# Kernel tuning notes

Hardware: AMD Instinct MI355X
Metric: run time of the kernel (lower is better)

## Reference

```python
import jax, jax.numpy as jnp
import numpy as np

H = 32  # GRU hidden size


def _conv1d(x, w, b, stride, pad):
    # x: (B, Cin, L), w: (Cout, Cin, K)
    y = jax.lax.conv_general_dilated(
        x, w, window_strides=(stride,), padding=[(pad, pad)],
        dimension_numbers=('NCH', 'OIH', 'NCH'))
    return y + b[None, :, None]


def setup_inputs() -> dict:
    key = jax.random.key(0)
    ks = jax.random.split(key, 16)
    B = 16384
    inp = {
        'past_samples': jax.random.normal(ks[0], (B, 2000), jnp.float32),
        'velocity': jax.random.uniform(ks[1], (B,), jnp.float32),
        'log_pitch': jax.random.normal(ks[2], (B,), jnp.float32),
        'time': jax.random.uniform(ks[3], (B,), jnp.float32),
        'hidden_state': jax.random.normal(ks[4], (B, H), jnp.float32),
        # conv stack params
        'w1': jax.random.normal(ks[5], (4, 1, 31), jnp.float32) * 0.1,
        'b1': jnp.zeros((4,), jnp.float32),
        'w2': jax.random.normal(ks[6], (8, 4, 15), jnp.float32) * 0.1,
        'b2': jnp.zeros((8,), jnp.float32),
        'w3': jax.random.normal(ks[7], (16, 8, 7), jnp.float32) * 0.1,
        'b3': jnp.zeros((16,), jnp.float32),
        # GRU params (torch layout: rows = [r; z; n])
        'w_ih': jax.random.normal(ks[8], (3 * H, 19), jnp.float32) * 0.1,
        'w_hh': jax.random.normal(ks[9], (3 * H, H), jnp.float32) * 0.1,
        'b_ih': jnp.zeros((3 * H,), jnp.float32),
        'b_hh': jnp.zeros((3 * H,), jnp.float32),
        # projection
        'w_proj': jax.random.normal(ks[10], (2, H), jnp.float32) * 0.1,
        'b_proj': jnp.zeros((2,), jnp.float32),
    }
    return inp


def reference(past_samples, velocity, log_pitch, time, hidden_state,
              w1, b1, w2, b2, w3, b3, w_ih, w_hh, b_ih, b_hh, w_proj, b_proj):
    x = past_samples[:, None, :]                       # (B,1,2000)
    x = jax.nn.relu(_conv1d(x, w1, b1, 4, 15))         # (B,4,500)
    x = jax.nn.relu(_conv1d(x, w2, b2, 4, 7))          # (B,8,125)
    x = jax.nn.relu(_conv1d(x, w3, b3, 4, 3))          # (B,16,32)
    ctx = jnp.mean(x, axis=2)                          # adaptive avg pool -> (B,16)

    rnn_in = jnp.concatenate(
        [ctx, velocity[:, None], log_pitch[:, None], time[:, None]], axis=1)  # (B,19)

    # single GRU step (torch GRUCell math)
    gi = rnn_in @ w_ih.T + b_ih                        # (B,3H)
    gh = hidden_state @ w_hh.T + b_hh                  # (B,3H)
    r = jax.nn.sigmoid(gi[:, :H] + gh[:, :H])
    z = jax.nn.sigmoid(gi[:, H:2 * H] + gh[:, H:2 * H])
    n = jnp.tanh(gi[:, 2 * H:] + r * gh[:, 2 * H:])
    new_hidden = (1.0 - z) * n + z * hidden_state      # (B,H)

    out = new_hidden @ w_proj.T + b_proj               # (B,2)
    mu, log_sigma = out[:, :1], out[:, 1:]
    sigma = jnp.exp(log_sigma)
    return (mu, sigma, new_hidden)
```

## Files before the change

### kernel.cpp

```cpp
#include <hip/hip_runtime.h>
#include <hip/hip_fp16.h>
#include <math.h>


typedef _Float16 h4 __attribute__((ext_vector_type(4)));
typedef _Float16 h8 __attribute__((ext_vector_type(8)));
typedef float f4 __attribute__((ext_vector_type(4)));

#define PACK_MAG0 0x57A9EDB1u
#define PACK_MAG1 0x1BDE9A75u
#define NITER 5

__device__ __forceinline__ void block_sync_lds()
{
    asm volatile("s_waitcnt lgkmcnt(0)" ::: "memory");
    __builtin_amdgcn_s_barrier();
}
__device__ __forceinline__ void wait_vm0()
{
    asm volatile("s_waitcnt vmcnt(0)" ::: "memory");
}

#if defined(__has_builtin)
#if __has_builtin(__builtin_amdgcn_global_load_lds)
#define HAVE_GLL 1
#endif
#endif

__device__ __forceinline__ void async_ld16(const float* g, float* lds)
{
#ifdef HAVE_GLL
    __builtin_amdgcn_global_load_lds(
        (const __attribute__((address_space(1))) void*)g,
        (__attribute__((address_space(3))) void*)lds, 16, 0, 0);
#else
    const int l = threadIdx.x & 63;
    ((float4*)lds)[l] = *(const float4*)g;
#endif
}

__global__ void pack_weights(const float* __restrict__ w1,
                             const float* __restrict__ w2,
                             const float* __restrict__ w3,
                             const float* __restrict__ w_ih,
                             _Float16* __restrict__ hws,
                             float* __restrict__ wihp,
                             unsigned int* __restrict__ flag)
{
    if (flag[0] == PACK_MAG0 && flag[1] == PACK_MAG1) return;

    for (int i = threadIdx.x; i < 1024; i += 256) {
        int kk = i >> 9, l = (i >> 3) & 63, j = i & 7;
        int m = l & 15, oct = l >> 4;
        int k = kk * 32 + oct * 8 + j;
        int delta = m >> 2, c = m & 3;
        int tap = k - 4 * delta - 1;
        float v = (tap >= 0 && tap < 31) ? w1[c * 31 + tap] : 0.0f;
        hws[i] = (_Float16)v;
    }
    for (int i = threadIdx.x; i < 1024; i += 256) {
        int kk = i >> 9, l = (i >> 3) & 63, j = i & 7;
        int c = l & 15, k = kk * 32 + ((l >> 4) << 3) + j;
        int tap = k >> 2, ci = k & 3;
        float v = (c < 8 && tap < 15) ? w2[(c * 4 + ci) * 15 + tap] : 0.0f;
        hws[1024 + i] = (_Float16)v;
    }
    for (int i = threadIdx.x; i < 1024; i += 256) {
        int kk = i >> 9, l = (i >> 3) & 63, j = i & 7;
        int c = l & 15, k = kk * 32 + ((l >> 4) << 3) + j;
        int tap = k >> 3, ci = k & 7;
        float v = (tap < 7) ? w3[(c * 8 + ci) * 7 + tap] : 0.0f;
        hws[2048 + i] = (_Float16)v;
    }
    for (int idx = threadIdx.x; idx < 96 * 20; idx += 256) {
        int r = idx / 20, c = idx % 20;
        wihp[idx] = (c < 19) ? w_ih[r * 19 + c] : 0.0f;
    }
    __syncthreads();
    if (threadIdx.x == 0) { flag[0] = PACK_MAG0; flag[1] = PACK_MAG1; }
}

__global__ void __launch_bounds__(128, 4)
wavernn_fused(const float* __restrict__ past,
              const float* __restrict__ velocity,
              const float* __restrict__ log_pitch,
              const float* __restrict__ time_in,
              const float* __restrict__ hidden,
              const float* __restrict__ b1,
              const float* __restrict__ b2,
              const float* __restrict__ b3,
              const float* __restrict__ wihp,
              const float* __restrict__ w_hh,
              const float* __restrict__ b_ih, const float* __restrict__ b_hh,
              const float* __restrict__ w_proj, const float* __restrict__ b_proj,
              const _Float16* __restrict__ hws,
              float* __restrict__ out, int B)
{
    __shared__ __align__(16) float regA[2048];
    __shared__ __align__(16) _Float16 regB[2112];
    __shared__ float rnnp[2][16];
    __shared__ float hsl[32];
    __shared__ float rnn3[4];

    float* const raw      = regA;
    _Float16* const y1t   = (_Float16*)regA;
    _Float16* const xbuf  = regB;
    _Float16* const y2t   = regB;
    float* const G        = (float*)regB;

    const h8* const wf1 = (const h8*)hws;
    const h8* const wf2 = (const h8*)(hws + 1024);
    const h8* const wf3 = (const h8*)(hws + 2048);

    const int tid = threadIdx.x;
    const int w   = tid >> 6;
    const int l   = tid & 63;
    const int o   = l >> 4;
    const int q   = l & 15;
    const f4 z4 = {0.0f, 0.0f, 0.0f, 0.0f};

    const int item0 = blockIdx.x * NITER;

    const h8 a10 = wf1[l],      a11 = wf1[64 + l];
    const h8 a20 = wf2[l],      a21 = wf2[64 + l];
    const h8 a30 = wf3[l],      a31 = wf3[64 + l];
    const float bv0 = b1[0], bv1 = b1[1], bv2 = b1[2], bv3 = b1[3];
    float b2v[4], b3v[4];
#pragma unroll
    for (int r = 0; r < 4; ++r) { b2v[r] = b2[(o * 4 + r) & 7];
                                  b3v[r] = b3[o * 4 + r]; }

    if (tid < 96) xbuf[2016 + tid] = (_Float16)0.0f;

    auto stage_issue = [&](int ii) {
        const float* row = past + (size_t)ii * 2000;
#pragma unroll
        for (int c = 0; c < 4; ++c) {
            int foff = w * 1024 + c * 256 + l * 4;
            if (foff > 1996) foff = 1996;
            async_ld16(row + foff, raw + w * 1024 + c * 256);
        }
    };

    stage_issue(item0);

    for (int it = 0; it < NITER; ++it) {
        const int ii = item0 + it;
        if (ii >= B) break;

        wait_vm0();
        if (tid < 32) hsl[tid] = hidden[(size_t)ii * 32 + tid];
        if (tid == 0) { rnn3[0] = velocity[ii];
                        rnn3[1] = log_pitch[ii];
                        rnn3[2] = time_in[ii]; }
        if (tid < 16) xbuf[tid] = (_Float16)0.0f;
        if (tid < 125) {
            const float4* r4 = (const float4*)raw + 4 * tid;
#pragma unroll
            for (int k = 0; k < 4; ++k) {
                float4 v = r4[k];
                h4 hv = {(_Float16)v.x, (_Float16)v.y,
                         (_Float16)v.z, (_Float16)v.w};
                *(h4*)(xbuf + 16 + 16 * tid + 4 * k) = hv;
            }
        }
        block_sync_lds();

        if (tid < 28) y1t[tid] = (_Float16)0.0f;
        else if (tid < 48) y1t[2000 + tid] = (_Float16)0.0f;
#pragma unroll
        for (int Ti = 0; Ti < 4; ++Ti) {
            const int T = 4 * w + Ti;
            h8 x0 = *(const h8*)(xbuf + 256 * T + 16 * q + 8 * o);
            h8 x1 = *(const h8*)(xbuf + 256 * T + 16 * q + 32 + 8 * o);
            f4 d = __builtin_amdgcn_mfma_f32_16x16x32_f16(a10, x0, z4, 0, 0, 0);
            d = __builtin_amdgcn_mfma_f32_16x16x32_f16(a11, x1, d, 0, 0, 0);
            const int p = 64 * T + 4 * q + o;
            if (p < 500) {
                h4 wv = {(_Float16)fmaxf(d[0] + bv0, 0.0f),
                         (_Float16)fmaxf(d[1] + bv1, 0.0f),
                         (_Float16)fmaxf(d[2] + bv2, 0.0f),
                         (_Float16)fmaxf(d[3] + bv3, 0.0f)};
                *(h4*)(y1t + (7 + p) * 4) = wv;
            }
        }
        block_sync_lds();

        if (tid < 24) y2t[tid] = (_Float16)0.0f;
        if (tid >= 96) y2t[928 + tid] = (_Float16)0.0f;
#pragma unroll
        for (int Ti = 0; Ti < 4; ++Ti) {
            const int T = 4 * w + Ti;
            const int p = T * 16 + q;
            h8 x0 = *(const h8*)(y1t + 16 * p + 8 * o);
            h8 x1 = *(const h8*)(y1t + 16 * p + 32 + 8 * o);
            f4 d = __builtin_amdgcn_mfma_f32_16x16x32_f16(a20, x0, z4, 0, 0, 0);
            d = __builtin_amdgcn_mfma_f32_16x16x32_f16(a21, x1, d, 0, 0, 0);
            if (o < 2 && p < 125) {
                h4 wv = {(_Float16)fmaxf(d[0] + b2v[0], 0.0f),
                         (_Float16)fmaxf(d[1] + b2v[1], 0.0f),
                         (_Float16)fmaxf(d[2] + b2v[2], 0.0f),
                         (_Float16)fmaxf(d[3] + b2v[3], 0.0f)};
                *(h4*)(y2t + (3 + p) * 8 + o * 4) = wv;
            }
        }
        block_sync_lds();

        if (it + 1 < NITER && ii + 1 < B) stage_issue(ii + 1);

        {
            const int p = 16 * w + q;
            h8 x0 = *(const h8*)(y2t + 32 * p + 8 * o);
            h8 x1 = *(const h8*)(y2t + 32 * p + 32 + 8 * o);
            f4 d = __builtin_amdgcn_mfma_f32_16x16x32_f16(a30, x0, z4, 0, 0, 0);
            d = __builtin_amdgcn_mfma_f32_16x16x32_f16(a31, x1, d, 0, 0, 0);
#pragma unroll
            for (int r = 0; r < 4; ++r) {
                float v = fmaxf(d[r] + b3v[r], 0.0f);
                v += __shfl_xor(v, 1); v += __shfl_xor(v, 2);
                v += __shfl_xor(v, 4); v += __shfl_xor(v, 8);
                if (q == 0) rnnp[w][o * 4 + r] = v;
            }
        }
        block_sync_lds();

        if (tid < 96) {
            float rv[20];
#pragma unroll
            for (int j = 0; j < 16; ++j)
                rv[j] = (rnnp[0][j] + rnnp[1][j]) * (1.0f / 32.0f);
            rv[16] = rnn3[0]; rv[17] = rnn3[1]; rv[18] = rnn3[2]; rv[19] = 0.0f;

            float a = b_ih[tid];
            const float4* wr = (const float4*)(wihp + tid * 20);
#pragma unroll
            for (int j = 0; j < 5; ++j) {
                float4 qv = wr[j];
                a += rv[4 * j] * qv.x + rv[4 * j + 1] * qv.y +
                     rv[4 * j + 2] * qv.z + rv[4 * j + 3] * qv.w;
            }
            G[tid] = a;

            float hv[32];
#pragma unroll
            for (int j = 0; j < 32; ++j) hv[j] = hsl[j];

            float g = b_hh[tid];
            const float4* wh = (const float4*)(w_hh + tid * 32);
#pragma unroll
            for (int j = 0; j < 8; ++j) {
                float4 qv = wh[j];
                g += hv[4 * j] * qv.x + hv[4 * j + 1] * qv.y +
                     hv[4 * j + 2] * qv.z + hv[4 * j + 3] * qv.w;
            }
            G[96 + tid] = g;
        }
        block_sync_lds();

        if (tid < 32) {
            const int j = tid;
            float r = 1.0f / (1.0f + expf(-(G[j] + G[96 + j])));
            float z = 1.0f / (1.0f + expf(-(G[32 + j] + G[128 + j])));
            float n = tanhf(G[64 + j] + r * G[160 + j]);
            float nh = (1.0f - z) * n + z * hsl[j];
            out[(size_t)2 * B + (size_t)ii * 32 + j] = nh;

            float p0 = nh * w_proj[j];
            float p1 = nh * w_proj[32 + j];
            p0 += __shfl_xor(p0, 16); p1 += __shfl_xor(p1, 16);
            p0 += __shfl_xor(p0, 8);  p1 += __shfl_xor(p1, 8);
            p0 += __shfl_xor(p0, 4);  p1 += __shfl_xor(p1, 4);
            p0 += __shfl_xor(p0, 2);  p1 += __shfl_xor(p1, 2);
            p0 += __shfl_xor(p0, 1);  p1 += __shfl_xor(p1, 1);
            if (j == 0) {
                out[ii] = p0 + b_proj[0];
                out[B + ii] = expf(p1 + b_proj[1]);
            }
        }
    }
}

extern "C" void kernel_launch(void* const* d_in, const int* in_sizes, int n_in,
                              void* d_out, int out_size, void* d_ws, size_t ws_size,
                              hipStream_t stream)
{
    const float* past      = (const float*)d_in[0];
    const float* velocity  = (const float*)d_in[1];
    const float* log_pitch = (const float*)d_in[2];
    const float* time_in   = (const float*)d_in[3];
    const float* hidden    = (const float*)d_in[4];
    const float* w1  = (const float*)d_in[5];
    const float* b1  = (const float*)d_in[6];
    const float* w2  = (const float*)d_in[7];
    const float* b2  = (const float*)d_in[8];
    const float* w3  = (const float*)d_in[9];
    const float* b3  = (const float*)d_in[10];
    const float* wih = (const float*)d_in[11];
    const float* whh = (const float*)d_in[12];
    const float* bih = (const float*)d_in[13];
    const float* bhh = (const float*)d_in[14];
    const float* wpr = (const float*)d_in[15];
    const float* bpr = (const float*)d_in[16];

    const int B = in_sizes[0] / 2000;
    _Float16* hws = (_Float16*)d_ws;
    float* wihp = (float*)((char*)d_ws + 8192);
    unsigned int* flag = (unsigned int*)((char*)d_ws + 16384);

    pack_weights<<<dim3(1), dim3(256), 0, stream>>>(w1, w2, w3, wih,
                                                    hws, wihp, flag);

    const int nblk = (B + NITER - 1) / NITER;
    wavernn_fused<<<dim3(nblk), dim3(128), 0, stream>>>(
        past, velocity, log_pitch, time_in, hidden,
        b1, b2, b3, wihp, whh, bih, bhh, wpr, bpr,
        (const _Float16*)hws, (float*)d_out, B);
}
```

Baseline: 278.1 us.

## Replace async global-to-LDS staging with register prefetch of next item

The global_load_lds staging buffer and its vmcnt wait are replaced by loading the next item's past samples, hidden state and scalars into registers, issued right after the current item is converted into the fp16 LDS buffer. y1t gets its own LDS array instead of aliasing the raw staging area, and G moves to its own array, so pad zeroing is hoisted out of the loop. The goal is to hide load latency across the whole conv/GRU body and remove a barrier. Items per block drop from 5 to 4, which raises block count. The trade-off is extra VGPRs for the prefetch registers under launch_bounds(128,4).

Measured after the change: 310.6 us. 1.12x slower.

```diff
diff --git a/kernel.cpp b/kernel.cpp
--- a/kernel.cpp
+++ b/kernel.cpp
@@ -9,34 +9,17 @@
 
 #define PACK_MAG0 0x57A9EDB1u
 #define PACK_MAG1 0x1BDE9A75u
-#define NITER 5
+#define NITER 4
 
 __device__ __forceinline__ void block_sync_lds()
 {
     asm volatile("s_waitcnt lgkmcnt(0)" ::: "memory");
     __builtin_amdgcn_s_barrier();
 }
-__device__ __forceinline__ void wait_vm0()
-{
-    asm volatile("s_waitcnt vmcnt(0)" ::: "memory");
-}
-
-#if defined(__has_builtin)
-#if __has_builtin(__builtin_amdgcn_global_load_lds)
-#define HAVE_GLL 1
-#endif
-#endif
-
-__device__ __forceinline__ void async_ld16(const float* g, float* lds)
-{
-#ifdef HAVE_GLL
-    __builtin_amdgcn_global_load_lds(
-        (const __attribute__((address_space(1))) void*)g,
-        (__attribute__((address_space(3))) void*)lds, 16, 0, 0);
-#else
-    const int l = threadIdx.x & 63;
-    ((float4*)lds)[l] = *(const float4*)g;
-#endif
+
+__device__ __forceinline__ h4 cvt4(float4 q)
+{
+    return (h4){(_Float16)q.x, (_Float16)q.y, (_Float16)q.z, (_Float16)q.w};
 }
 
 __global__ void pack_weights(const float* __restrict__ w1,
@@ -96,17 +79,15 @@
               const _Float16* __restrict__ hws,
               float* __restrict__ out, int B)
 {
-    __shared__ __align__(16) float regA[2048];
     __shared__ __align__(16) _Float16 regB[2112];
+    __shared__ __align__(16) _Float16 y1t[2048];
+    __shared__ float G[192];
     __shared__ float rnnp[2][16];
     __shared__ float hsl[32];
     __shared__ float rnn3[4];
 
-    float* const raw      = regA;
-    _Float16* const y1t   = (_Float16*)regA;
-    _Float16* const xbuf  = regB;
-    _Float16* const y2t   = regB;
-    float* const G        = (float*)regB;
+    _Float16* const xbuf = regB;
+    _Float16* const y2t  = regB;
 
     const h8* const wf1 = (const h8*)hws;
     const h8* const wf2 = (const h8*)(hws + 1024);
@@ -131,43 +112,41 @@
                                   b3v[r] = b3[o * 4 + r]; }
 
     if (tid < 96) xbuf[2016 + tid] = (_Float16)0.0f;
-
-    auto stage_issue = [&](int ii) {
-        const float* row = past + (size_t)ii * 2000;
-#pragma unroll
-        for (int c = 0; c < 4; ++c) {
-            int foff = w * 1024 + c * 256 + l * 4;
-            if (foff > 1996) foff = 1996;
-            async_ld16(row + foff, raw + w * 1024 + c * 256);
-        }
+    if (tid < 28) y1t[tid] = (_Float16)0.0f;
+    else if (tid < 48) y1t[2000 + tid] = (_Float16)0.0f;
+
+    float4 pf[4];
+    float hn = 0.0f, sn = 0.0f;
+    auto issue_item_loads = [&](int ii) {
+        const float4* row4 = (const float4*)(past + (size_t)ii * 2000);
+#pragma unroll
+        for (int j = 0; j < 4; ++j) {
+            int i = tid + 128 * j;
+            pf[j] = row4[i < 500 ? i : 499];
+        }
+        if (tid < 32) hn = hidden[(size_t)ii * 32 + tid];
+        if (tid == 0) sn = velocity[ii];
+        if (tid == 1) sn = log_pitch[ii];
+        if (tid == 2) sn = time_in[ii];
     };
 
-    stage_issue(item0);
+    issue_item_loads(item0);
 
     for (int it = 0; it < NITER; ++it) {
         const int ii = item0 + it;
         if (ii >= B) break;
 
-        wait_vm0();
-        if (tid < 32) hsl[tid] = hidden[(size_t)ii * 32 + tid];
-        if (tid == 0) { rnn3[0] = velocity[ii];
-                        rnn3[1] = log_pitch[ii];
-                        rnn3[2] = time_in[ii]; }
+        if (tid < 32) hsl[tid] = hn;
+        if (tid < 3)  rnn3[tid] = sn;
         if (tid < 16) xbuf[tid] = (_Float16)0.0f;
-        if (tid < 125) {
-            const float4* r4 = (const float4*)raw + 4 * tid;
-#pragma unroll
-            for (int k = 0; k < 4; ++k) {
-                float4 v = r4[k];
-                h4 hv = {(_Float16)v.x, (_Float16)v.y,
-                         (_Float16)v.z, (_Float16)v.w};
-                *(h4*)(xbuf + 16 + 16 * tid + 4 * k) = hv;
-            }
-        }
-        block_sync_lds();
-
-        if (tid < 28) y1t[tid] = (_Float16)0.0f;
-        else if (tid < 48) y1t[2000 + tid] = (_Float16)0.0f;
+#pragma unroll
+        for (int j = 0; j < 4; ++j) {
+            int i = tid + 128 * j;
+            if (i < 500) *(h4*)(xbuf + 16 + 4 * i) = cvt4(pf[j]);
+        }
+        if (it + 1 < NITER && ii + 1 < B) issue_item_loads(ii + 1);
+        block_sync_lds();
+
 #pragma unroll
         for (int Ti = 0; Ti < 4; ++Ti) {
             const int T = 4 * w + Ti;
@@ -205,8 +184,6 @@
             }
         }
         block_sync_lds();
-
-        if (it + 1 < NITER && ii + 1 < B) stage_issue(ii + 1);
 
         {
             const int p = 16 * w + q;
```
